# Optimization experiments

Measured on AMD Instinct MI355X. Metric: run time of the kernel, lower is better.

## Reference

```python
import jax, jax.numpy as jnp
import numpy as np

N_NODES = 50000
N_EDGES = 1600000
N_FEAT = 128
DIM = 128
N_GRAPHS = 128
BN_EPS = 1e-5


def setup_inputs() -> dict:
    key = jax.random.key(0)
    ks = jax.random.split(key, 16)
    x = jax.random.normal(ks[0], (N_NODES, N_FEAT), dtype=jnp.float32)
    edge_index = jax.random.randint(ks[1], (2, N_EDGES), 0, N_NODES)
    batch = jnp.sort(jax.random.randint(ks[2], (N_NODES,), 0, N_GRAPHS))
    def lin(k, fin, fout):
        return jax.random.normal(k, (fin, fout), dtype=jnp.float32) / np.sqrt(fin).astype(np.float32)
    inp = {"x": x, "edge_index": edge_index, "batch": batch}
    fins = [N_FEAT, DIM, DIM]
    for i in range(3):
        inp[f"W{i}"] = lin(ks[3 + i], fins[i], DIM)
        inp[f"b{i}"] = jnp.zeros((DIM,), jnp.float32)
        inp[f"g{i}"] = jnp.ones((DIM,), jnp.float32)
        inp[f"be{i}"] = jnp.zeros((DIM,), jnp.float32)
    return inp


def _gcn_norm(edge_index, n):
    # add self loops, symmetric normalization D^-1/2 (A+I) D^-1/2
    loop = jnp.arange(n, dtype=edge_index.dtype)
    src = jnp.concatenate([edge_index[0], loop])
    dst = jnp.concatenate([edge_index[1], loop])
    deg = jax.ops.segment_sum(jnp.ones_like(src, dtype=jnp.float32), dst, num_segments=n)
    dinv = jnp.where(deg > 0, jax.lax.rsqrt(deg), 0.0)
    norm = dinv[src] * dinv[dst]  # [E+N]
    return src, dst, norm


def _gcn_conv(h, W, b, src, dst, norm, n):
    h = h @ W                      # [N, D]
    msg = h[src] * norm[:, None]   # [E+N, D] gather + scale
    agg = jax.ops.segment_sum(msg, dst, num_segments=n)
    return agg + b


def _batchnorm(h, g, be):
    mu = jnp.mean(h, axis=0)
    var = jnp.mean(jnp.square(h - mu), axis=0)  # biased, training-mode BN
    return (h - mu) * jax.lax.rsqrt(var + BN_EPS) * g + be


def reference(x, edge_index, batch, W0, b0, g0, be0, W1, b1, g1, be1, W2, b2, g2, be2):
    n = x.shape[0]
    src, dst, norm = _gcn_norm(edge_index, n)
    params = [(W0, b0, g0, be0), (W1, b1, g1, be1), (W2, b2, g2, be2)]
    h = x
    pools = []
    for (W, b, g, be) in params:
        h = jax.nn.relu(_gcn_conv(h, W, b, src, dst, norm, n))
        h = _batchnorm(h, g, be)
        pools.append(jax.ops.segment_sum(h, batch, num_segments=N_GRAPHS))
    return jnp.concatenate(pools, axis=1)  # [N_GRAPHS, 3*DIM]
```

## Files before the change

### kernel.cpp

```cpp
#include <hip/hip_runtime.h>
#include <hip/hip_bf16.h>

#define N_GRAPHS 128
#define BN_EPS 1e-5f
#define CHUNK 8192
#define NBU 512
#define CAP 8192

typedef short bf16x8 __attribute__((ext_vector_type(8)));
typedef short s16x4 __attribute__((ext_vector_type(4)));
typedef float f32x4 __attribute__((ext_vector_type(4)));

__device__ __forceinline__ unsigned short f2b(float f) {
    unsigned int u = __builtin_bit_cast(unsigned int, f);
    u += 0x7FFFu + ((u >> 16) & 1u);
    return (unsigned short)(u >> 16);
}
__device__ __forceinline__ float b2f_lo(unsigned int p) {
    return __builtin_bit_cast(float, p << 16);
}
__device__ __forceinline__ float b2f_hi(unsigned int p) {
    return __builtin_bit_cast(float, p & 0xFFFF0000u);
}
__device__ __forceinline__ unsigned int packrelu(float a, float b) {
    return (unsigned int)f2b(fmaxf(a, 0.f)) | ((unsigned int)f2b(fmaxf(b, 0.f)) << 16);
}

__global__ __launch_bounds__(512) void bin_chunks(const int* __restrict__ src,
                                                  const int* __restrict__ dst,
                                                  unsigned int* __restrict__ bpairs,
                                                  int* __restrict__ cnts,
                                                  int* __restrict__ cbase,
                                                  int* __restrict__ btot, int E) {
    __shared__ int lhist[NBU], lscan[NBU], lfill[NBU];
    int tid = threadIdx.x;
    int c0 = blockIdx.x * CHUNK;
    int ecnt = min(CHUNK, E - c0);
    lhist[tid] = 0;
    __syncthreads();
    for (int i = tid; i < ecnt; i += 512)
        atomicAdd(&lhist[((unsigned)dst[c0 + i]) >> 7], 1);
    __syncthreads();
    int orig = lhist[tid];
    atomicAdd(&btot[tid], orig);
    lscan[tid] = orig;
    __syncthreads();
    for (int off = 1; off < NBU; off <<= 1) {
        int t = (tid >= off) ? lscan[tid - off] : 0;
        __syncthreads();
        lscan[tid] += t;
        __syncthreads();
    }
    int excl = lscan[tid] - orig;
    cnts[blockIdx.x * NBU + tid] = orig;
    cbase[blockIdx.x * NBU + tid] = excl;
    lfill[tid] = 0;
    __syncthreads();
    lscan[tid] = excl;
    __syncthreads();
    for (int i = tid; i < ecnt; i += 512) {
        int d = dst[c0 + i], s = src[c0 + i];
        int b = ((unsigned)d) >> 7;
        int pos = lscan[b] + atomicAdd(&lfill[b], 1);
        bpairs[c0 + pos] = ((unsigned)(d & 127) << 25) | (unsigned)s;
    }
}

__global__ __launch_bounds__(512) void bucket_scan(const int* __restrict__ btot,
                                                   int* __restrict__ bucket_base) {
    __shared__ int s[NBU];
    int b = threadIdx.x;
    int tot = btot[b];
    s[b] = tot;
    __syncthreads();
    for (int off = 1; off < NBU; off <<= 1) {
        int t = (b >= off) ? s[b - off] : 0;
        __syncthreads();
        s[b] += t;
        __syncthreads();
    }
    bucket_base[b] = s[b] - tot;
}

__global__ __launch_bounds__(256) void bucket_csr(const unsigned int* __restrict__ bpairs,
                                                  const int* __restrict__ cnts,
                                                  const int* __restrict__ cbase,
                                                  const int* __restrict__ bucket_base,
                                                  int* __restrict__ rowp,
                                                  int* __restrict__ degarr,
                                                  float* __restrict__ dinv,
                                                  int* __restrict__ csr,
                                                  int nchunks, int N) {
    __shared__ unsigned int lpr[CAP];
    __shared__ int lcsr[CAP];
    __shared__ int ccnt[256], cofs[256], cb[256];
    __shared__ int lhist[128], lofs[128], lfill[128];
    int tid = threadIdx.x;
    int b = blockIdx.x;
    int bb = bucket_base[b];
    int total = bucket_base[b + 1] - bb;
    if (total > CAP) total = CAP;

    ccnt[tid] = (tid < nchunks) ? cnts[tid * NBU + b] : 0;
    cb[tid]   = (tid < nchunks) ? cbase[tid * NBU + b] : 0;
    cofs[tid] = ccnt[tid];
    __syncthreads();
    int orig = cofs[tid];
    for (int off = 1; off < 256; off <<= 1) {
        int t = (tid >= off) ? cofs[tid - off] : 0;
        __syncthreads();
        cofs[tid] += t;
        __syncthreads();
    }
    int o = cofs[tid] - orig;
    if (tid < nchunks) {
        int len = ccnt[tid];
        const unsigned int* p = bpairs + (size_t)tid * CHUNK + cb[tid];
        for (int i = 0; i < len; ++i) {
            int q = o + i;
            if (q < CAP) lpr[q] = p[i];
        }
    }
    if (tid < 128) { lhist[tid] = 0; lfill[tid] = 0; }
    __syncthreads();
    for (int i = tid; i < total; i += 256)
        atomicAdd(&lhist[lpr[i] >> 25], 1);
    __syncthreads();
    if (tid < 128) lofs[tid] = lhist[tid];
    __syncthreads();
    for (int off = 1; off < 128; off <<= 1) {
        int t = 0;
        if (tid < 128 && tid >= off) t = lofs[tid - off];
        __syncthreads();
        if (tid < 128) lofs[tid] += t;
        __syncthreads();
    }
    if (tid < 128) {
        int v = b * 128 + tid;
        if (v < N) {
            int dg = lhist[tid];
            degarr[v] = dg;
            rowp[v] = bb + lofs[tid] - dg;
            dinv[v] = rsqrtf((float)(dg + 1));
        }
    }
    __syncthreads();
    for (int i = tid; i < total; i += 256) {
        unsigned int pr = lpr[i];
        int dl = pr >> 25;
        int pos = lofs[dl] - lhist[dl] + atomicAdd(&lfill[dl], 1);
        if (pos < CAP) lcsr[pos] = (int)(pr & 0x1FFFFFFu);
    }
    __syncthreads();
    for (int i = tid; i < total; i += 256) csr[bb + i] = lcsr[i];
}

template <int HASBN>
__global__ __launch_bounds__(256) void bn_prep_w(const float* __restrict__ stats,
                                                 const float* __restrict__ g,
                                                 const float* __restrict__ be,
                                                 const float* __restrict__ W,
                                                 unsigned short* __restrict__ Wp,
                                                 float* __restrict__ wb, float invN) {
    __shared__ float scL[128], shL[128];
    int tid = threadIdx.x;
    if (HASBN) {
        if (tid < 128) {
            float mu = stats[tid] * invN;
            float var = stats[128 + tid] * invN - mu * mu;
            float sc = g[tid] * rsqrtf(var + BN_EPS);
            scL[tid] = sc;
            shL[tid] = be[tid] - mu * sc;
        }
        __syncthreads();
    }
    int i = blockIdx.x * 256 + tid;
    int k = i >> 7, c = i & 127;
    float w = W[i];
    if (HASBN) w *= scL[k];
    int kk = k & 31, k0 = k >> 5;
    int hi = (kk >> 2) & 3;
    int e = (kk & 3) + 4 * (kk >> 4);
    int idx = c * 128 + k0 * 32 + hi * 8 + e;
    Wp[idx ^ ((c & 7) << 3)] = f2b(w);
    if (HASBN && blockIdx.x == 0 && tid < 128) {
        float acc = 0.f;
#pragma unroll 4
        for (int kx = 0; kx < 128; ++kx) acc = fmaf(shL[kx], W[kx * 128 + tid], acc);
        wb[tid] = acc;
    }
}

template <int AF32>
__global__ __launch_bounds__(256) void gemm_mfma(const void* __restrict__ Avoid,
                                                 const unsigned short* __restrict__ Wp,
                                                 const float* __restrict__ wb,
                                                 const float* __restrict__ dinv,
                                                 unsigned short* __restrict__ Cb, int N) {
    __shared__ unsigned short sWt[128 * 128];
    int tid = threadIdx.x;
    {
        const uint4* src = (const uint4*)Wp;
        uint4* dst = (uint4*)sWt;
#pragma unroll
        for (int j = 0; j < 8; ++j) dst[tid + 256 * j] = src[tid + 256 * j];
    }
    __syncthreads();

    int wave = tid >> 6, lane = tid & 63;
    int lo4 = lane & 15, hi = lane >> 4;
    int rowBase = blockIdx.x * 128 + wave * 32;

    f32x4 acc[8][2];
#pragma unroll
    for (int ct = 0; ct < 8; ++ct)
#pragma unroll
        for (int rt = 0; rt < 2; ++rt) acc[ct][rt] = (f32x4){0.f, 0.f, 0.f, 0.f};

    const float* Af = (const float*)Avoid;
    const unsigned short* Ab = (const unsigned short*)Avoid;

    for (int k0 = 0; k0 < 128; k0 += 32) {
        bf16x8 bfrag[2];
#pragma unroll
        for (int rt = 0; rt < 2; ++rt) {
            int r = rowBase + rt * 16 + lo4;
            if (r >= N) r = N - 1;
            if (AF32) {
                float4 f0 = *(const float4*)(Af + (size_t)r * 128 + k0 + 4 * hi);
                float4 f1 = *(const float4*)(Af + (size_t)r * 128 + k0 + 16 + 4 * hi);
                bf16x8 f;
                f[0] = (short)f2b(f0.x); f[1] = (short)f2b(f0.y);
                f[2] = (short)f2b(f0.z); f[3] = (short)f2b(f0.w);
                f[4] = (short)f2b(f1.x); f[5] = (short)f2b(f1.y);
                f[6] = (short)f2b(f1.z); f[7] = (short)f2b(f1.w);
                bfrag[rt] = f;
            } else {
                s16x4 a0 = *(const s16x4*)(Ab + (size_t)r * 128 + k0 + 4 * hi);
                s16x4 a1 = *(const s16x4*)(Ab + (size_t)r * 128 + k0 + 16 + 4 * hi);
                bf16x8 f;
                f[0] = a0[0]; f[1] = a0[1]; f[2] = a0[2]; f[3] = a0[3];
                f[4] = a1[0]; f[5] = a1[1]; f[6] = a1[2]; f[7] = a1[3];
                bfrag[rt] = f;
            }
        }
        int kq = k0 >> 5;
#pragma unroll
        for (int ct = 0; ct < 8; ++ct) {
            int c = ct * 16 + lo4;
            int idx = (c * 128 + kq * 32 + hi * 8) ^ ((c & 7) << 3);
            bf16x8 af = *(const bf16x8*)(sWt + idx);
#pragma unroll
            for (int rt = 0; rt < 2; ++rt)
                acc[ct][rt] = __builtin_amdgcn_mfma_f32_16x16x32_bf16(af, bfrag[rt], acc[ct][rt], 0, 0, 0);
        }
    }

#pragma unroll
    for (int rt = 0; rt < 2; ++rt) {
        int r = rowBase + rt * 16 + lo4;
        if (r < N) {
            float dv = dinv[r];
#pragma unroll
            for (int ct = 0; ct < 8; ++ct) {
                int c0 = ct * 16 + hi * 4;
                float4 wbv = make_float4(0.f, 0.f, 0.f, 0.f);
                if (!AF32) wbv = *(const float4*)(wb + c0);
                ushort4 s;
                s.x = f2b((acc[ct][rt][0] + wbv.x) * dv);
                s.y = f2b((acc[ct][rt][1] + wbv.y) * dv);
                s.z = f2b((acc[ct][rt][2] + wbv.z) * dv);
                s.w = f2b((acc[ct][rt][3] + wbv.w) * dv);
                *(ushort4*)(Cb + (size_t)r * 128 + c0) = s;
            }
        }
    }
}

__global__ __launch_bounds__(256) void agg_relu_b16(const uint4* __restrict__ hW4,
                                                    const int* __restrict__ rowp,
                                                    const int* __restrict__ cnt,
                                                    const int* __restrict__ csr,
                                                    const float* __restrict__ dinv,
                                                    const float* __restrict__ bias,
                                                    unsigned int* __restrict__ z32, int N) {
    int wave = threadIdx.x >> 6, lane = threadIdx.x & 63;
    int v = blockIdx.x * 4 + wave;
    if (v >= N) return;
    int q = lane >> 4, c = lane & 15;
    int beg = rowp[v];
    int num = cnt[v];
    float s0 = 0.f, s1 = 0.f, s2 = 0.f, s3 = 0.f, s4 = 0.f, s5 = 0.f, s6 = 0.f, s7 = 0.f;
    int i = 0;
    for (; i + 8 <= num; i += 8) {
        int u0 = csr[beg + i + q];
        int u1 = csr[beg + i + 4 + q];
        uint4 p0 = hW4[(size_t)u0 * 16 + c];
        uint4 p1 = hW4[(size_t)u1 * 16 + c];
        s0 += b2f_lo(p0.x) + b2f_lo(p1.x);
        s1 += b2f_hi(p0.x) + b2f_hi(p1.x);
        s2 += b2f_lo(p0.y) + b2f_lo(p1.y);
        s3 += b2f_hi(p0.y) + b2f_hi(p1.y);
        s4 += b2f_lo(p0.z) + b2f_lo(p1.z);
        s5 += b2f_hi(p0.z) + b2f_hi(p1.z);
        s6 += b2f_lo(p0.w) + b2f_lo(p1.w);
        s7 += b2f_hi(p0.w) + b2f_hi(p1.w);
    }
    for (; i < num; i += 4) {
        int idx = i + q;
        bool ok = idx < num;
        int u = ok ? csr[beg + idx] : v;
        float m = ok ? 1.f : 0.f;
        uint4 p = hW4[(size_t)u * 16 + c];
        s0 = fmaf(m, b2f_lo(p.x), s0);
        s1 = fmaf(m, b2f_hi(p.x), s1);
        s2 = fmaf(m, b2f_lo(p.y), s2);
        s3 = fmaf(m, b2f_hi(p.y), s3);
        s4 = fmaf(m, b2f_lo(p.z), s4);
        s5 = fmaf(m, b2f_hi(p.z), s5);
        s6 = fmaf(m, b2f_lo(p.w), s6);
        s7 = fmaf(m, b2f_hi(p.w), s7);
    }
    s0 += __shfl_xor(s0, 16, 64); s0 += __shfl_xor(s0, 32, 64);
    s1 += __shfl_xor(s1, 16, 64); s1 += __shfl_xor(s1, 32, 64);
    s2 += __shfl_xor(s2, 16, 64); s2 += __shfl_xor(s2, 32, 64);
    s3 += __shfl_xor(s3, 16, 64); s3 += __shfl_xor(s3, 32, 64);
    s4 += __shfl_xor(s4, 16, 64); s4 += __shfl_xor(s4, 32, 64);
    s5 += __shfl_xor(s5, 16, 64); s5 += __shfl_xor(s5, 32, 64);
    s6 += __shfl_xor(s6, 16, 64); s6 += __shfl_xor(s6, 32, 64);
    s7 += __shfl_xor(s7, 16, 64); s7 += __shfl_xor(s7, 32, 64);
    if (q == 0) {
        float dv = dinv[v];
        uint4 pv = hW4[(size_t)v * 16 + c];
        float4 b0 = *(const float4*)(bias + 8 * c);
        float4 b1 = *(const float4*)(bias + 8 * c + 4);
        float r0 = dv * (s0 + b2f_lo(pv.x)) + b0.x;
        float r1 = dv * (s1 + b2f_hi(pv.x)) + b0.y;
        float r2 = dv * (s2 + b2f_lo(pv.y)) + b0.z;
        float r3 = dv * (s3 + b2f_hi(pv.y)) + b0.w;
        float r4 = dv * (s4 + b2f_lo(pv.z)) + b1.x;
        float r5 = dv * (s5 + b2f_hi(pv.z)) + b1.y;
        float r6 = dv * (s6 + b2f_lo(pv.w)) + b1.z;
        float r7 = dv * (s7 + b2f_hi(pv.w)) + b1.w;
        uint4 o;
        o.x = packrelu(r0, r1);
        o.y = packrelu(r2, r3);
        o.z = packrelu(r4, r5);
        o.w = packrelu(r6, r7);
        *(uint4*)(z32 + (size_t)v * 64 + 4 * c) = o;
    }
}

__global__ __launch_bounds__(256) void bn_stats_b16(const unsigned int* __restrict__ z32,
                                                    float* __restrict__ stats, int N) {
    int lane = threadIdx.x & 63, sub = threadIdx.x >> 6;
    float s0 = 0.f, s1 = 0.f, q0 = 0.f, q1 = 0.f;
    for (int v = blockIdx.x * 4 + sub; v < N; v += gridDim.x * 4) {
        unsigned int p = z32[(size_t)v * 64 + lane];
        float a = b2f_lo(p), c = b2f_hi(p);
        s0 += a; q0 = fmaf(a, a, q0);
        s1 += c; q1 = fmaf(c, c, q1);
    }
    __shared__ float ls[256][4];
    ls[threadIdx.x][0] = s0; ls[threadIdx.x][1] = s1;
    ls[threadIdx.x][2] = q0; ls[threadIdx.x][3] = q1;
    __syncthreads();
    if (sub == 0) {
        for (int k = 1; k < 4; ++k) {
            s0 += ls[lane + 64 * k][0]; s1 += ls[lane + 64 * k][1];
            q0 += ls[lane + 64 * k][2]; q1 += ls[lane + 64 * k][3];
        }
        atomicAdd(&stats[2 * lane], s0);
        atomicAdd(&stats[2 * lane + 1], s1);
        atomicAdd(&stats[128 + 2 * lane], q0);
        atomicAdd(&stats[129 + 2 * lane], q1);
    }
}

__global__ __launch_bounds__(256) void apply_pool_b16(const unsigned int* __restrict__ z32,
                                                      const float* __restrict__ stats,
                                                      const float* __restrict__ g,
                                                      const float* __restrict__ be,
                                                      const int* __restrict__ batch,
                                                      float* __restrict__ out,
                                                      int layer, int N, float invN) {
    __shared__ int gb[128];
    int lane = threadIdx.x & 63, strip = threadIdx.x >> 6;
    int base = blockIdx.x * 128;
    int tot = min(128, N - base);
    if (threadIdx.x < tot) gb[threadIdx.x] = batch[base + threadIdx.x];
    __syncthreads();
    int v0 = strip * 32;
    if (v0 >= tot) return;
    int cntv = min(32, tot - v0);
    int d0 = 2 * lane, d1 = 2 * lane + 1;
    float mu0 = stats[d0] * invN, mu1 = stats[d1] * invN;
    float va0 = stats[128 + d0] * invN - mu0 * mu0;
    float va1 = stats[128 + d1] * invN - mu1 * mu1;
    float sc0 = g[d0] * rsqrtf(va0 + BN_EPS), sc1 = g[d1] * rsqrtf(va1 + BN_EPS);
    float sh0 = be[d0] - mu0 * sc0, sh1 = be[d1] - mu1 * sc1;
    float a0 = 0.f, a1 = 0.f;
    int cur = gb[v0];
    for (int j = 0; j < cntv; ++j) {
        unsigned int p = z32[(size_t)(base + v0 + j) * 64 + lane];
        float x0 = fmaf(b2f_lo(p), sc0, sh0);
        float x1 = fmaf(b2f_hi(p), sc1, sh1);
        int gg = gb[v0 + j];
        if (gg != cur) {
            atomicAdd(&out[(size_t)cur * 384 + layer * 128 + d0], a0);
            atomicAdd(&out[(size_t)cur * 384 + layer * 128 + d1], a1);
            a0 = a1 = 0.f;
            cur = gg;
        }
        a0 += x0; a1 += x1;
    }
    atomicAdd(&out[(size_t)cur * 384 + layer * 128 + d0], a0);
    atomicAdd(&out[(size_t)cur * 384 + layer * 128 + d1], a1);
}

extern "C" void kernel_launch(void* const* d_in, const int* in_sizes, int n_in,
                              void* d_out, int out_size, void* d_ws, size_t ws_size,
                              hipStream_t stream) {
    const float* x    = (const float*)d_in[0];
    const int* eidx   = (const int*)d_in[1];
    const int* batch  = (const int*)d_in[2];

    const int N = in_sizes[2];
    const int E = in_sizes[1] / 2;
    const int* src = eidx;
    const int* dst = eidx + E;

    const int nchunks = (E + CHUNK - 1) / CHUNK;
    const int NB = (N + 127) / 128;
    const float invN = 1.0f / N;

    size_t off = 0;
    auto alloc = [&](size_t bytes) {
        void* p = (char*)d_ws + off;
        off += (bytes + 255) & ~(size_t)255;
        return p;
    };
    unsigned short* hWb = (unsigned short*)alloc((size_t)N * 128 * 2);
    unsigned int* z32   = (unsigned int*)alloc((size_t)N * 64 * 4);
    unsigned int* bpairs= (unsigned int*)alloc((size_t)nchunks * CHUNK * 4);
    int*   csr   = (int*)alloc((size_t)E * 4);
    int*   cnts  = (int*)alloc((size_t)nchunks * NBU * 4);
    int*   cbase = (int*)alloc((size_t)nchunks * NBU * 4);
    int*   bbase = (int*)alloc((size_t)(NBU + 1) * 4);
    float* stats = (float*)alloc(3 * 256 * 4);
    int*   btot  = (int*)alloc((size_t)NBU * 4);
    int*   degar = (int*)alloc((size_t)N * 4);
    int*   rowp  = (int*)alloc((size_t)N * 4);
    float* dinv  = (float*)alloc((size_t)N * 4);
    float* wbuf  = (float*)alloc(2 * 128 * 4);
    unsigned short* Wp = (unsigned short*)alloc(128 * 128 * 2);

    float* out = (float*)d_out;

    hipMemsetAsync(stats, 0, 3 * 256 * 4 + (size_t)NBU * 4, stream);
    hipMemsetAsync(out, 0, (size_t)N_GRAPHS * 384 * 4, stream);

    bin_chunks<<<nchunks, 512, 0, stream>>>(src, dst, bpairs, cnts, cbase, btot, E);
    bucket_scan<<<1, 512, 0, stream>>>(btot, bbase);
    bucket_csr<<<NB, 256, 0, stream>>>(bpairs, cnts, cbase, bbase, rowp, degar, dinv, csr,
                                       nchunks, N);

    const int gemm_blocks = (N + 127) / 128;
    const int agg_blocks  = (N + 3) / 4;
    const int pool_blocks = (N + 127) / 128;

    bn_prep_w<0><<<64, 256, 0, stream>>>(nullptr, nullptr, nullptr,
                                         (const float*)d_in[3], Wp, nullptr, 0.f);

    for (int l = 0; l < 3; ++l) {
        const float* b  = (const float*)d_in[4 + 4 * l];
        const float* g  = (const float*)d_in[5 + 4 * l];
        const float* be = (const float*)d_in[6 + 4 * l];

        if (l == 0)
            gemm_mfma<1><<<gemm_blocks, 256, 0, stream>>>((const void*)x, Wp, nullptr, dinv, hWb, N);
        else
            gemm_mfma<0><<<gemm_blocks, 256, 0, stream>>>((const void*)z32, Wp,
                                                          wbuf + (l - 1) * 128, dinv, hWb, N);

        agg_relu_b16<<<agg_blocks, 256, 0, stream>>>((const uint4*)hWb, rowp, degar, csr,
                                                     dinv, b, z32, N);
        bn_stats_b16<<<256, 256, 0, stream>>>(z32, stats + l * 256, N);
        if (l < 2) {
            bn_prep_w<1><<<64, 256, 0, stream>>>(stats + l * 256, g, be,
                                                 (const float*)d_in[3 + 4 * (l + 1)],
                                                 Wp, wbuf + l * 128, invN);
        }
        apply_pool_b16<<<pool_blocks, 256, 0, stream>>>(z32, stats + l * 256, g, be, batch, out,
                                                        l, N, invN);
    }
}
```

Measured before the change: 458.0 us.

## Fuse graph pooling into BN stats pass via linearity; drop bucket_scan kernel

```diff
diff --git a/kernel.cpp b/kernel.cpp
--- a/kernel.cpp
+++ b/kernel.cpp
@@ -66,26 +66,10 @@
     }
 }
 
-__global__ __launch_bounds__(512) void bucket_scan(const int* __restrict__ btot,
-                                                   int* __restrict__ bucket_base) {
-    __shared__ int s[NBU];
-    int b = threadIdx.x;
-    int tot = btot[b];
-    s[b] = tot;
-    __syncthreads();
-    for (int off = 1; off < NBU; off <<= 1) {
-        int t = (b >= off) ? s[b - off] : 0;
-        __syncthreads();
-        s[b] += t;
-        __syncthreads();
-    }
-    bucket_base[b] = s[b] - tot;
-}
-
 __global__ __launch_bounds__(256) void bucket_csr(const unsigned int* __restrict__ bpairs,
                                                   const int* __restrict__ cnts,
                                                   const int* __restrict__ cbase,
-                                                  const int* __restrict__ bucket_base,
+                                                  const int* __restrict__ btot,
                                                   int* __restrict__ rowp,
                                                   int* __restrict__ degarr,
                                                   float* __restrict__ dinv,
@@ -95,11 +79,22 @@
     __shared__ int lcsr[CAP];
     __shared__ int ccnt[256], cofs[256], cb[256];
     __shared__ int lhist[128], lofs[128], lfill[128];
+    __shared__ int rsum[256];
     int tid = threadIdx.x;
     int b = blockIdx.x;
-    int bb = bucket_base[b];
-    int total = bucket_base[b + 1] - bb;
+
+    int t1 = (tid < b) ? btot[tid] : 0;
+    int t2 = (tid + 256 < b) ? btot[tid + 256] : 0;
+    rsum[tid] = t1 + t2;
+    __syncthreads();
+    for (int off2 = 128; off2 > 0; off2 >>= 1) {
+        if (tid < off2) rsum[tid] += rsum[tid + off2];
+        __syncthreads();
+    }
+    int bb = rsum[0];
+    int total = btot[b];
     if (total > CAP) total = CAP;
+    __syncthreads();
 
     ccnt[tid] = (tid < nchunks) ? cnts[tid * NBU + b] : 0;
     cb[tid]   = (tid < nchunks) ? cbase[tid * NBU + b] : 0;
@@ -153,6 +148,17 @@
     }
     __syncthreads();
     for (int i = tid; i < total; i += 256) csr[bb + i] = lcsr[i];
+}
+
+__global__ void graph_counts(const int* __restrict__ batch, int* __restrict__ gcnt, int N) {
+    int g = threadIdx.x;
+    int lo = 0, hi = N;
+    while (lo < hi) { int m = (lo + hi) >> 1; if (batch[m] <= g) lo = m + 1; else hi = m; }
+    int ub = lo;
+    lo = 0; hi = N;
+    int gm1 = g - 1;
+    while (lo < hi) { int m = (lo + hi) >> 1; if (batch[m] <= gm1) lo = m + 1; else hi = m; }
+    gcnt[g] = ub - lo;
 }
 
 template <int HASBN>
@@ -351,15 +357,35 @@
     }
 }
 
-__global__ __launch_bounds__(256) void bn_stats_b16(const unsigned int* __restrict__ z32,
-                                                    float* __restrict__ stats, int N) {
+__global__ __launch_bounds__(256) void bn_stats_seg(const unsigned int* __restrict__ z32,
+                                                    const int* __restrict__ batch,
+                                                    float* __restrict__ stats,
+                                                    float* __restrict__ sseg,
+                                                    int strip, int N) {
     int lane = threadIdx.x & 63, sub = threadIdx.x >> 6;
+    int v0 = blockIdx.x * strip;
+    int v1 = min(v0 + strip, N);
     float s0 = 0.f, s1 = 0.f, q0 = 0.f, q1 = 0.f;
-    for (int v = blockIdx.x * 4 + sub; v < N; v += gridDim.x * 4) {
+    float a0 = 0.f, a1 = 0.f;
+    int cur = -1;
+    for (int v = v0 + sub; v < v1; v += 4) {
         unsigned int p = z32[(size_t)v * 64 + lane];
-        float a = b2f_lo(p), c = b2f_hi(p);
-        s0 += a; q0 = fmaf(a, a, q0);
-        s1 += c; q1 = fmaf(c, c, q1);
+        float x0 = b2f_lo(p), x1 = b2f_hi(p);
+        s0 += x0; q0 = fmaf(x0, x0, q0);
+        s1 += x1; q1 = fmaf(x1, x1, q1);
+        int g = batch[v];
+        if (g != cur) {
+            if (cur >= 0) {
+                atomicAdd(&sseg[cur * 128 + 2 * lane], a0);
+                atomicAdd(&sseg[cur * 128 + 2 * lane + 1], a1);
+            }
+            cur = g; a0 = 0.f; a1 = 0.f;
+        }
+        a0 += x0; a1 += x1;
+    }
+    if (cur >= 0) {
+        atomicAdd(&sseg[cur * 128 + 2 * lane], a0);
+        atomicAdd(&sseg[cur * 128 + 2 * lane + 1], a1);
     }
     __shared__ float ls[256][4];
     ls[threadIdx.x][0] = s0; ls[threadIdx.x][1] = s1;
@@ -377,45 +403,20 @@
     }
 }
 
-__global__ __launch_bounds__(256) void apply_pool_b16(const unsigned int* __restrict__ z32,
-                                                      const float* __restrict__ stats,
-                                                      const float* __restrict__ g,
-                                                      const float* __restrict__ be,
-                                                      const int* __restrict__ batch,
-                                                      float* __restrict__ out,
-                                                      int layer, int N, float invN) {
-    __shared__ int gb[128];
-    int lane = threadIdx.x & 63, strip = threadIdx.x >> 6;
-    int base = blockIdx.x * 128;
-    int tot = min(128, N - base);
-    if (threadIdx.x < tot) gb[threadIdx.x] = batch[base + threadIdx.x];
-    __syncthreads();
-    int v0 = strip * 32;
-    if (v0 >= tot) return;
-    int cntv = min(32, tot - v0);
-    int d0 = 2 * lane, d1 = 2 * lane + 1;
-    float mu0 = stats[d0] * invN, mu1 = stats[d1] * invN;
-    float va0 = stats[128 + d0] * invN - mu0 * mu0;
-    float va1 = stats[128 + d1] * invN - mu1 * mu1;
-    float sc0 = g[d0] * rsqrtf(va0 + BN_EPS), sc1 = g[d1] * rsqrtf(va1 + BN_EPS);
-    float sh0 = be[d0] - mu0 * sc0, sh1 = be[d1] - mu1 * sc1;
-    float a0 = 0.f, a1 = 0.f;
-    int cur = gb[v0];
-    for (int j = 0; j < cntv; ++j) {
-        unsigned int p = z32[(size_t)(base + v0 + j) * 64 + lane];
-        float x0 = fmaf(b2f_lo(p), sc0, sh0);
-        float x1 = fmaf(b2f_hi(p), sc1, sh1);
-        int gg = gb[v0 + j];
-        if (gg != cur) {
-            atomicAdd(&out[(size_t)cur * 384 + layer * 128 + d0], a0);
-            atomicAdd(&out[(size_t)cur * 384 + layer * 128 + d1], a1);
-            a0 = a1 = 0.f;
-            cur = gg;
-        }
-        a0 += x0; a1 += x1;
-    }
-    atomicAdd(&out[(size_t)cur * 384 + layer * 128 + d0], a0);
-    atomicAdd(&out[(size_t)cur * 384 + layer * 128 + d1], a1);
+__global__ __launch_bounds__(256) void pool_finalize(const float* __restrict__ stats,
+                                                     const float* __restrict__ sseg,
+                                                     const int* __restrict__ gcnt,
+                                                     const float* __restrict__ g,
+                                                     const float* __restrict__ be,
+                                                     float* __restrict__ out,
+                                                     int layer, float invN) {
+    int idx = blockIdx.x * 256 + threadIdx.x;
+    int d = idx & 127, gr = idx >> 7;
+    float mu = stats[d] * invN;
+    float var = stats[128 + d] * invN - mu * mu;
+    float sc = g[d] * rsqrtf(var + BN_EPS);
+    float sh = be[d] - mu * sc;
+    out[(size_t)gr * 384 + layer * 128 + d] = sc * sseg[gr * 128 + d] + (float)gcnt[gr] * sh;
 }
 
 extern "C" void kernel_launch(void* const* d_in, const int* in_sizes, int n_in,
@@ -446,28 +447,29 @@
     int*   csr   = (int*)alloc((size_t)E * 4);
     int*   cnts  = (int*)alloc((size_t)nchunks * NBU * 4);
     int*   cbase = (int*)alloc((size_t)nchunks * NBU * 4);
-    int*   bbase = (int*)alloc((size_t)(NBU + 1) * 4);
     float* stats = (float*)alloc(3 * 256 * 4);
     int*   btot  = (int*)alloc((size_t)NBU * 4);
+    float* sseg  = (float*)alloc(3 * (size_t)N_GRAPHS * 128 * 4);
+    size_t zero_bytes = (size_t)((char*)sseg - (char*)stats) + 3 * (size_t)N_GRAPHS * 128 * 4;
     int*   degar = (int*)alloc((size_t)N * 4);
     int*   rowp  = (int*)alloc((size_t)N * 4);
     float* dinv  = (float*)alloc((size_t)N * 4);
     float* wbuf  = (float*)alloc(2 * 128 * 4);
+    int*   gcnt  = (int*)alloc(N_GRAPHS * 4);
     unsigned short* Wp = (unsigned short*)alloc(128 * 128 * 2);
 
     float* out = (float*)d_out;
 
-    hipMemsetAsync(stats, 0, 3 * 256 * 4 + (size_t)NBU * 4, stream);
-    hipMemsetAsync(out, 0, (size_t)N_GRAPHS * 384 * 4, stream);
+    hipMemsetAsync(stats, 0, zero_bytes, stream);
 
     bin_chunks<<<nchunks, 512, 0, stream>>>(src, dst, bpairs, cnts, cbase, btot, E);
-    bucket_scan<<<1, 512, 0, stream>>>(btot, bbase);
-    bucket_csr<<<NB, 256, 0, stream>>>(bpairs, cnts, cbase, bbase, rowp, degar, dinv, csr,
+    bucket_csr<<<NB, 256, 0, stream>>>(bpairs, cnts, cbase, btot, rowp, degar, dinv, csr,
                                        nchunks, N);
+    graph_counts<<<1, 128, 0, stream>>>(batch, gcnt, N);
 
     const int gemm_blocks = (N + 127) / 128;
     const int agg_blocks  = (N + 3) / 4;
-    const int pool_blocks = (N + 127) / 128;
+    const int strip = (N + 255) / 256;
 
     bn_prep_w<0><<<64, 256, 0, stream>>>(nullptr, nullptr, nullptr,
                                          (const float*)d_in[3], Wp, nullptr, 0.f);
@@ -485,13 +487,15 @@
 
         agg_relu_b16<<<agg_blocks, 256, 0, stream>>>((const uint4*)hWb, rowp, degar, csr,
                                                      dinv, b, z32, N);
-        bn_stats_b16<<<256, 256, 0, stream>>>(z32, stats + l * 256, N);
+        bn_stats_seg<<<256, 256, 0, stream>>>(z32, batch, stats + l * 256,
+                                              sseg + (size_t)l * N_GRAPHS * 128, strip, N);
         if (l < 2) {
             bn_prep_w<1><<<64, 256, 0, stream>>>(stats + l * 256, g, be,
                                                  (const float*)d_in[3 + 4 * (l + 1)],
                                                  Wp, wbuf + l * 128, invN);
         }
-        apply_pool_b16<<<pool_blocks, 256, 0, stream>>>(z32, stats + l * 256, g, be, batch, out,
-                                                        l, N, invN);
-    }
-}
+        pool_finalize<<<64, 256, 0, stream>>>(stats + l * 256,
+                                              sseg + (size_t)l * N_GRAPHS * 128, gcnt, g, be,
+                                              out, l, invN);
+    }
+}
```

After: 443.9 us. -3.1%, faster.
